# Kernel optimization log

Hardware: AMD Instinct MI355X
Metric: run time of the kernel (lower is better)

## Reference

```python
import jax, jax.numpy as jnp
import numpy as np

B, T, D = 4, 4096, 1024
H = 16
DK = D // H
EPS = 1e-6


def _phi(x):
    return jax.nn.elu(x) + 1.0


def setup_inputs() -> dict:
    key = jax.random.key(0)
    ks = jax.random.split(key, 9)
    s = 1.0 / np.sqrt(D)
    return {
        "x": jax.random.normal(ks[0], (B, T, D), dtype=jnp.float32),
        "Wq": jax.random.uniform(ks[1], (D, D), jnp.float32, -s, s),
        "bq": jax.random.uniform(ks[2], (D,), jnp.float32, -s, s),
        "Wk": jax.random.uniform(ks[3], (D, D), jnp.float32, -s, s),
        "bk": jax.random.uniform(ks[4], (D,), jnp.float32, -s, s),
        "Wv": jax.random.uniform(ks[5], (D, D), jnp.float32, -s, s),
        "bv": jax.random.uniform(ks[6], (D,), jnp.float32, -s, s),
        "Wo": jax.random.uniform(ks[7], (D, D), jnp.float32, -s, s),
        "bo": jax.random.uniform(ks[8], (D,), jnp.float32, -s, s),
    }


def reference(x, Wq, bq, Wk, bk, Wv, bv, Wo, bo):
    Bq, Tq, _ = x.shape

    def heads(y):  # [B,T,D] -> [B,H,T,DK]
        return y.reshape(Bq, Tq, H, DK).transpose(0, 2, 1, 3)

    q = _phi(heads(x @ Wq.T + bq))
    k = _phi(heads(x @ Wk.T + bk))
    v = heads(x @ Wv.T + bv)

    # associative KV summary: [B,H,DK,DK]
    kv = jnp.einsum("bhtd,bhtm->bhdm", k, v)
    # normalizer: q . (sum_t k + eps), then +eps, reciprocal
    z = 1.0 / (jnp.einsum("bhtd,bhd->bht", q, k.sum(axis=2) + EPS) + EPS)
    out = jnp.einsum("bhtd,bhdm,bht->bhtm", q, kv, z)

    out = out.transpose(0, 2, 1, 3).reshape(Bq, Tq, -1)  # [B,T,D]
    return out @ Wo.T + bo
```

## Files before the change

kernel.cpp:

```cpp
#include <hip/hip_runtime.h>
#include <cstdint>
#include <cstddef>

typedef unsigned short u16;
typedef __bf16 bf16x8 __attribute__((ext_vector_type(8)));
typedef float  f32x4  __attribute__((ext_vector_type(4)));
typedef u16    u16x8v __attribute__((ext_vector_type(8)));
typedef u16    u16x4  __attribute__((ext_vector_type(4)));

#define EPS 1e-6f

__device__ __forceinline__ u16 f2bf(float f) {
  union { float f; unsigned int u; } v; v.f = f;
  unsigned int u = v.u + 0x7FFFu + ((v.u >> 16) & 1u);
  return (u16)(u >> 16);
}
__device__ __forceinline__ float bf2f(u16 h) {
  union { unsigned int u; float f; } v; v.u = ((unsigned int)h) << 16;
  return v.f;
}
__device__ __forceinline__ void async16(const void* g, void* l) {
  __builtin_amdgcn_global_load_lds(
      (const __attribute__((address_space(1))) void*)g,
      (__attribute__((address_space(3))) void*)l, 16, 0, 0);
}

__global__ __launch_bounds__(256) void cvt_bf16_kernel(
    const float* __restrict__ in, u16* __restrict__ out, int n8) {
  int i = blockIdx.x * 256 + threadIdx.x;
  if (i >= n8) return;
  const float4* p = (const float4*)in;
  float4 a = p[2 * (size_t)i], b = p[2 * (size_t)i + 1];
  u16x8v o;
  o[0] = f2bf(a.x); o[1] = f2bf(a.y); o[2] = f2bf(a.z); o[3] = f2bf(a.w);
  o[4] = f2bf(b.x); o[5] = f2bf(b.y); o[6] = f2bf(b.z); o[7] = f2bf(b.w);
  *(u16x8v*)(out + 8 * (size_t)i) = o;
}

__global__ __launch_bounds__(256) void cvt_w_kernel(
    const float* __restrict__ w0, const float* __restrict__ w1,
    const float* __restrict__ w2, const float* __restrict__ w3,
    u16* __restrict__ o0, u16* __restrict__ o1,
    u16* __restrict__ o2, u16* __restrict__ o3) {
  const int gb = blockIdx.x;
  const float* in = (gb < 512) ? w0 : (gb < 1024) ? w1 : (gb < 1536) ? w2 : w3;
  u16* out = (gb < 512) ? o0 : (gb < 1024) ? o1 : (gb < 1536) ? o2 : o3;
  const int i = (gb & 511) * 256 + threadIdx.x;
  const float4* p = (const float4*)in;
  float4 a = p[2 * (size_t)i], b = p[2 * (size_t)i + 1];
  u16x8v o;
  o[0] = f2bf(a.x); o[1] = f2bf(a.y); o[2] = f2bf(a.z); o[3] = f2bf(a.w);
  o[4] = f2bf(b.x); o[5] = f2bf(b.y); o[6] = f2bf(b.z); o[7] = f2bf(b.w);
  *(u16x8v*)(out + 8 * (size_t)i) = o;
}

template <int MODE>
__global__ __launch_bounds__(512) void gemm2p(
    const u16* __restrict__ A, const u16* __restrict__ Bw,
    const float* __restrict__ bias0, const float* __restrict__ bias1,
    const float* __restrict__ bias2,
    u16* __restrict__ O0, u16* __restrict__ O1, u16* __restrict__ O2,
    float* __restrict__ Of, int K) {
  __shared__ u16 sA[2][256 * 64];
  __shared__ u16 sB[2][256 * 64];

  const int tid  = threadIdx.x;
  const int wave = tid >> 6;
  const int lane = tid & 63;
  const int bm = blockIdx.x * 256;
  const int bn = blockIdx.y * 256;
  const int wm = (wave >> 2) * 128;
  const int wn = (wave & 3) * 64;

  f32x4 acc[8][4] = {};

  const int srow = tid >> 3;
  const int sch8 = ((tid & 7) ^ ((tid >> 3) & 7)) * 8;
  const u16* gA0 = A  + (size_t)(bm + srow) * K + sch8;
  const u16* gB0 = Bw + (size_t)(bn + srow) * K + sch8;
  const int dwb = wave * 8 * 64;

#define STAGE2P(buf, k0)                                           \
  {                                                                \
    _Pragma("unroll")                                              \
    for (int s = 0; s < 4; s++) {                                  \
      async16(gA0 + (size_t)(k0) + (size_t)s * 64 * K,             \
              &sA[buf][s * 64 * 64 + dwb]);                        \
      async16(gB0 + (size_t)(k0) + (size_t)s * 64 * K,             \
              &sB[buf][s * 64 * 64 + dwb]);                        \
    }                                                              \
  }

  const int l15 = lane & 15, l4 = lane >> 4, l7 = lane & 7;

  STAGE2P(0, 0);
  __syncthreads();

  int cur = 0;
  const int NT = K >> 6;
  for (int t = 0; t < NT; ++t) {
    if (t + 1 < NT) STAGE2P(cur ^ 1, (t + 1) * 64);
#pragma unroll
    for (int kk = 0; kk < 2; kk++) {
      const int slot = ((kk * 4 + l4) ^ l7) * 8;
      bf16x8 af[8], bfv[4];
#pragma unroll
      for (int i = 0; i < 8; i++)
        af[i] = *(const bf16x8*)&sA[cur][(wm + i * 16 + l15) * 64 + slot];
#pragma unroll
      for (int n = 0; n < 4; n++)
        bfv[n] = *(const bf16x8*)&sB[cur][(wn + n * 16 + l15) * 64 + slot];
#pragma unroll
      for (int mi = 0; mi < 8; mi++)
#pragma unroll
        for (int ni = 0; ni < 4; ni++)
          acc[mi][ni] = __builtin_amdgcn_mfma_f32_16x16x32_bf16(
              af[mi], bfv[ni], acc[mi][ni], 0, 0, 0);
    }
    __syncthreads();
    cur ^= 1;
  }
#undef STAGE2P

  const int r0 = (lane >> 4) * 4, cc = lane & 15;
  if constexpr (MODE == 1) {
    const int mat = blockIdx.y >> 2;
    u16* outp = (mat == 0) ? O0 : (mat == 1) ? O1 : O2;
    const float* bias = (mat == 0) ? bias0 : (mat == 1) ? bias1 : bias2;
    const int act = (mat < 2);
    const int colb = (blockIdx.y & 3) * 256;
#pragma unroll
    for (int ni = 0; ni < 4; ni++) {
      const int col = colb + wn + ni * 16 + cc;
      const float bv = bias[col];
#pragma unroll
      for (int mi = 0; mi < 8; mi++) {
#pragma unroll
        for (int j = 0; j < 4; j++) {
          const int row = bm + wm + mi * 16 + r0 + j;
          float val = acc[mi][ni][j] + bv;
          if (act) val = (val > 0.f) ? (val + 1.f) : __expf(val);
          outp[(size_t)row * 1024 + col] = f2bf(val);
        }
      }
    }
  } else {
#pragma unroll
    for (int ni = 0; ni < 4; ni++) {
      const int col = bn + wn + ni * 16 + cc;
      const float bv = bias0[col];
#pragma unroll
      for (int mi = 0; mi < 8; mi++) {
#pragma unroll
        for (int j = 0; j < 4; j++) {
          const int row = bm + wm + mi * 16 + r0 + j;
          Of[(size_t)row * 1024 + col] = acc[mi][ni][j] + bv;
        }
      }
    }
  }
}

__global__ __launch_bounds__(256) void kv_mfma_kernel(
    const u16* __restrict__ Kb, const u16* __restrict__ Vb,
    float* __restrict__ kv, float* __restrict__ ksum) {
  const int bh = blockIdx.y;
  const int chunk = blockIdx.x;
  const int b = bh >> 4, h = bh & 15;
  const int tid = threadIdx.x, wave = tid >> 6, lane = tid & 63;

  __shared__ u16 sKT[64 * 64];
  __shared__ u16 sVT[64 * 64];

  f32x4 acc[4] = {};
  f32x4 accs[4] = {};

  union { u16x8v u; bf16x8 b; } uo;
#pragma unroll
  for (int e = 0; e < 8; e++) uo.u[e] = 0x3F80;
  const bf16x8 ones = uo.b;

  const int half = tid >> 7;
  const int j    = tid & 127;
  const int tg   = j >> 3;
  const int dg   = j & 7;
  const u16* src = half ? Vb : Kb;
  u16* dst = half ? sVT : sKT;
  const int colb = (4 * tg + 8 * dg) & 63;

  const size_t rowBase = (size_t)b * 4096 + (size_t)chunk * 512;
  const size_t gbase = (rowBase + 4 * tg) * 1024 + (size_t)h * 64 + dg * 8;

  u16x8v pre[2][4];
#pragma unroll
  for (int s = 0; s < 4; s++)
    pre[0][s] = *(const u16x8v*)(src + gbase + (size_t)s * 1024);

#pragma unroll
  for (int st = 0; st < 8; st++) {
    const int cb = st & 1;
    __syncthreads();
#pragma unroll
    for (int e = 0; e < 8; e++) {
      u16x4 w;
      w[0] = pre[cb][0][e]; w[1] = pre[cb][1][e];
      w[2] = pre[cb][2][e]; w[3] = pre[cb][3][e];
      *(u16x4*)&dst[(dg * 8 + e) * 64 + colb] = w;
    }
    if (st + 1 < 8) {
      const size_t nb = gbase + (size_t)(st + 1) * 64 * 1024;
#pragma unroll
      for (int s = 0; s < 4; s++)
        pre[cb ^ 1][s] = *(const u16x8v*)(src + nb + (size_t)s * 1024);
    }
    __syncthreads();

#pragma unroll
    for (int kst = 0; kst < 2; kst++) {
      const int q8 = kst * 32 + (lane >> 4) * 8;
      bf16x8 bfrag;
      {
        const int rr = wave * 16 + (lane & 15);
        const int c = (q8 + 8 * (rr >> 3)) & 63;
        bfrag = *(const bf16x8*)&sVT[rr * 64 + c];
      }
#pragma unroll
      for (int i = 0; i < 4; i++) {
        const int rr = i * 16 + (lane & 15);
        const int c = (q8 + 8 * (rr >> 3)) & 63;
        const bf16x8 afrag = *(const bf16x8*)&sKT[rr * 64 + c];
        acc[i] = __builtin_amdgcn_mfma_f32_16x16x32_bf16(afrag, bfrag, acc[i], 0, 0, 0);
        if (wave == 0)
          accs[i] = __builtin_amdgcn_mfma_f32_16x16x32_bf16(afrag, ones, accs[i], 0, 0, 0);
      }
    }
  }

  const int r0 = (lane >> 4) * 4, cc = lane & 15;
  float* kvp = kv + (size_t)bh * 4096;
#pragma unroll
  for (int i = 0; i < 4; i++)
#pragma unroll
    for (int jj = 0; jj < 4; jj++)
      atomicAdd(&kvp[(size_t)(i * 16 + r0 + jj) * 64 + wave * 16 + cc], acc[i][jj]);
  if (wave == 0 && cc == 0) {
#pragma unroll
    for (int i = 0; i < 4; i++)
#pragma unroll
      for (int jj = 0; jj < 4; jj++)
        atomicAdd(&ksum[(size_t)bh * 64 + i * 16 + r0 + jj], accs[i][jj]);
  }
}

#define QST 80
__global__ __launch_bounds__(256) void attn_apply_kernel(
    const u16* __restrict__ Qb, const float* __restrict__ kv,
    const float* __restrict__ ksum, u16* __restrict__ attn) {
  const int bh = blockIdx.y;
  const int tt = blockIdx.x;
  const int b = bh >> 4, h = bh & 15;
  const int tid = threadIdx.x, wave = tid >> 6, lane = tid & 63;

  __shared__ u16 skvT[64 * QST];
  __shared__ u16 sq[64 * QST];
  __shared__ float sz[64];
  __shared__ float sks[64];

  if (tid < 64) sks[tid] = ksum[(size_t)bh * 64 + tid] + EPS;

  const float* kvp = kv + (size_t)bh * 4096;
  for (int i = tid; i < 4096; i += 256) {
    const int dd = i >> 6, mm = i & 63;
    skvT[mm * QST + dd] = f2bf(kvp[i]);
  }
  const size_t qbase = ((size_t)b * 4096 + (size_t)tt * 64) * 1024 + h * 64;
  for (int i = tid; i < 4096; i += 256) {
    const int r = i >> 6, dd = i & 63;
    sq[r * QST + dd] = Qb[qbase + (size_t)r * 1024 + dd];
  }
  __syncthreads();

  if (tid < 64) {
    float za = 0.f;
#pragma unroll
    for (int j = 0; j < 64; j++) {
      const int dd = (j + tid) & 63;
      za += bf2f(sq[tid * QST + dd]) * sks[dd];
    }
    sz[tid] = 1.f / (za + EPS);
  }
  __syncthreads();

  f32x4 acc[4] = {};
#pragma unroll
  for (int ks2 = 0; ks2 < 2; ks2++) {
    const bf16x8 a = *(const bf16x8*)&sq[(wave * 16 + (lane & 15)) * QST + ks2 * 32 + (lane >> 4) * 8];
#pragma unroll
    for (int ni = 0; ni < 4; ni++) {
      const bf16x8 bv = *(const bf16x8*)&skvT[(ni * 16 + (lane & 15)) * QST + ks2 * 32 + (lane >> 4) * 8];
      acc[ni] = __builtin_amdgcn_mfma_f32_16x16x32_bf16(a, bv, acc[ni], 0, 0, 0);
    }
  }

  const int r0 = (lane >> 4) * 4, cc = lane & 15;
#pragma unroll
  for (int ni = 0; ni < 4; ni++) {
#pragma unroll
    for (int j = 0; j < 4; j++) {
      const int r = wave * 16 + r0 + j;
      const int c = ni * 16 + cc;
      const float val = acc[ni][j] * sz[r];
      attn[qbase + (size_t)r * 1024 + c] = f2bf(val);
    }
  }
}

extern "C" void kernel_launch(void* const* d_in, const int* in_sizes, int n_in,
                              void* d_out, int out_size, void* d_ws, size_t ws_size,
                              hipStream_t stream) {
  (void)in_sizes; (void)n_in; (void)out_size; (void)ws_size;
  const float* x  = (const float*)d_in[0];
  const float* Wq = (const float*)d_in[1];
  const float* bq = (const float*)d_in[2];
  const float* Wk = (const float*)d_in[3];
  const float* bk = (const float*)d_in[4];
  const float* Wv = (const float*)d_in[5];
  const float* bv = (const float*)d_in[6];
  const float* Wo = (const float*)d_in[7];
  const float* bo = (const float*)d_in[8];

  char* ws = (char*)d_ws;
  u16* xb    = (u16*)ws;  ws += 33554432;
  u16* wqkvb = (u16*)ws;  ws += 6291456;
  u16* wob   = (u16*)ws;  ws += 2097152;
  u16* Vb    = (u16*)ws;  ws += 33554432;
  u16* attn  = (u16*)ws;  ws += 33554432;
  float* kvb  = (float*)ws; ws += 1048576;
  float* ksum = (float*)ws; ws += 16384;

  u16* Qb = (u16*)d_out;
  u16* Kb = Qb + 16777216;

  hipMemsetAsync(kvb, 0, 1048576 + 16384, stream);

  cvt_bf16_kernel<<<8192, 256, 0, stream>>>(x, xb, 2097152);
  cvt_w_kernel<<<2048, 256, 0, stream>>>(Wq, Wk, Wv, Wo,
                                         wqkvb, wqkvb + 1048576, wqkvb + 2097152, wob);

  gemm2p<1><<<dim3(64, 12), 512, 0, stream>>>(
      xb, wqkvb, bq, bk, bv, Qb, Kb, Vb, nullptr, 1024);

  kv_mfma_kernel<<<dim3(8, 64), dim3(256), 0, stream>>>(Kb, Vb, kvb, ksum);
  attn_apply_kernel<<<dim3(64, 64), dim3(256), 0, stream>>>(Qb, kvb, ksum, attn);

  gemm2p<0><<<dim3(64, 4), 512, 0, stream>>>(
      attn, wob, bo, nullptr, nullptr, nullptr, nullptr, nullptr,
      (float*)d_out, 1024);
}
```

Baseline: 367.4 us.

## Rewrite GEMM main loop as 8-phase quadrant pipeline with interleaved async loads

Replaces the double-buffered GEMM loop with an 8-phase schedule. Each 256x256 tile is split into quadrant sub-tiles, and async global-to-LDS loads for the next k-steps are spread between the MFMA phases, with explicit vmcnt waits, barriers and setprio around MFMA bursts. The aim is to hide global load latency and reduce LDS read stalls by keeping fewer fragments live and overlapping loads with compute. It also changes the wave-to-tile mapping and reorders the epilogue stores. This adds complex hand-managed synchronization that could stall or be wrong if the wait counts are off, and it assumes K is a multiple of 128.

```diff
diff --git a/kernel.cpp b/kernel.cpp
--- a/kernel.cpp
+++ b/kernel.cpp
@@ -55,7 +55,7 @@
 }
 
 template <int MODE>
-__global__ __launch_bounds__(512) void gemm2p(
+__global__ __launch_bounds__(512) void gemm8p(
     const u16* __restrict__ A, const u16* __restrict__ Bw,
     const float* __restrict__ bias0, const float* __restrict__ bias1,
     const float* __restrict__ bias2,
@@ -64,97 +64,144 @@
   __shared__ u16 sA[2][256 * 64];
   __shared__ u16 sB[2][256 * 64];
 
-  const int tid  = threadIdx.x;
-  const int wave = tid >> 6;
-  const int lane = tid & 63;
-  const int bm = blockIdx.x * 256;
-  const int bn = blockIdx.y * 256;
-  const int wm = (wave >> 2) * 128;
+  const int tid = threadIdx.x, wave = tid >> 6, lane = tid & 63;
+  const int bm = blockIdx.x * 256, bn = blockIdx.y * 256;
+  const int wmh = (wave >> 2) * 64;
+  const int wq  = (wave & 3) * 32;
+  const int l15 = lane & 15, l4 = lane >> 4, l7 = lane & 7;
+
+  f32x4 acc[8][4] = {};
+
+  const int trow = tid >> 3;
+  const int sch8 = ((tid & 7) ^ (trow & 7)) * 8;
+
+#define STG_A(buf, qm, s, kt)                                                 \
+  async16(A + (size_t)(bm + (s)*128 + (qm)*64 + trow) * K + (kt) + sch8,      \
+          &sA[buf][(((qm)*128 + (s)*64) + wave * 8) * 64])
+#define STG_B(buf, qn, s, kt)                                                 \
+  async16(Bw + (size_t)(bn + ((s)*2 + (trow >> 5)) * 64 + (qn)*32 +           \
+                        (trow & 31)) * K + (kt) + sch8,                       \
+          &sB[buf][(((qn)*128 + (s)*64) + wave * 8) * 64])
+
+  bf16x8 af[4][2], bq[2][2];
+
+#define PH_READS(buf, qm, qn)                                                 \
+  _Pragma("unroll") for (int m = 0; m < 4; m++)                               \
+    _Pragma("unroll") for (int kk = 0; kk < 2; kk++)                          \
+      af[m][kk] = *(const bf16x8*)&sA[buf][((qm)*128 + wmh + m * 16 + l15) * 64 \
+                                           + ((kk * 4 + l4) ^ l7) * 8];       \
+  _Pragma("unroll") for (int n = 0; n < 2; n++)                               \
+    _Pragma("unroll") for (int kk = 0; kk < 2; kk++)                          \
+      bq[n][kk] = *(const bf16x8*)&sB[buf][((qn)*128 + wq + n * 16 + l15) * 64 \
+                                           + ((kk * 4 + l4) ^ l7) * 8];
+
+#define PH_MFMA(qm, qn)                                                       \
+  __builtin_amdgcn_s_barrier();                                               \
+  asm volatile("s_waitcnt lgkmcnt(0)" ::: "memory");                          \
+  __builtin_amdgcn_s_setprio(1);                                              \
+  _Pragma("unroll") for (int kk = 0; kk < 2; kk++)                            \
+    _Pragma("unroll") for (int m = 0; m < 4; m++)                             \
+      _Pragma("unroll") for (int n = 0; n < 2; n++)                           \
+        acc[(qm)*4 + m][(qn)*2 + n] = __builtin_amdgcn_mfma_f32_16x16x32_bf16(\
+            af[m][kk], bq[n][kk], acc[(qm)*4 + m][(qn)*2 + n], 0, 0, 0);      \
+  __builtin_amdgcn_s_setprio(0);                                              \
+  __builtin_amdgcn_s_barrier();                                               \
+  asm volatile("" ::: "memory");
+
+  STG_A(0, 0, 0, 0);  STG_A(0, 0, 1, 0);
+  STG_B(0, 0, 0, 0);  STG_B(0, 0, 1, 0);
+  STG_A(0, 1, 0, 0);  STG_A(0, 1, 1, 0);
+  STG_B(0, 1, 0, 0);  STG_B(0, 1, 1, 0);
+  STG_A(1, 0, 0, 64); STG_A(1, 0, 1, 64);
+  STG_B(1, 0, 0, 64); STG_B(1, 0, 1, 64);
+  asm volatile("s_waitcnt vmcnt(4)" ::: "memory");
+  __builtin_amdgcn_s_barrier();
+  asm volatile("" ::: "memory");
+
+  const int NT = K >> 6;
+  const int NI = NT >> 1;
+  for (int i = 0; i < NI; ++i) {
+    const int kO  = (2 * i + 1) * 64;
+    const int kE2 = (2 * i + 2) * 64;
+    const int kO2 = (2 * i + 3) * 64;
+    const bool gE2 = (2 * i + 2) < NT;
+    const bool gO2 = (2 * i + 3) < NT;
+
+    PH_READS(0, 0, 0);
+    STG_A(1, 1, 0, kO); STG_A(1, 1, 1, kO);
+    PH_MFMA(0, 0);
+    PH_READS(0, 0, 1);
+    STG_B(1, 1, 0, kO); STG_B(1, 1, 1, kO);
+    PH_MFMA(0, 1);
+    PH_READS(0, 1, 0);
+    if (gE2) { STG_A(0, 0, 0, kE2); STG_A(0, 0, 1, kE2); }
+    PH_MFMA(1, 0);
+    PH_READS(0, 1, 1);
+    if (gE2) {
+      STG_B(0, 0, 0, kE2); STG_B(0, 0, 1, kE2);
+      asm volatile("s_waitcnt vmcnt(4)" ::: "memory");
+    } else {
+      asm volatile("s_waitcnt vmcnt(0)" ::: "memory");
+    }
+    PH_MFMA(1, 1);
+    PH_READS(1, 0, 0);
+    if (gE2) { STG_A(0, 1, 0, kE2); STG_A(0, 1, 1, kE2); }
+    PH_MFMA(0, 0);
+    PH_READS(1, 0, 1);
+    if (gE2) { STG_B(0, 1, 0, kE2); STG_B(0, 1, 1, kE2); }
+    PH_MFMA(0, 1);
+    PH_READS(1, 1, 0);
+    if (gO2) { STG_A(1, 0, 0, kO2); STG_A(1, 0, 1, kO2); }
+    PH_MFMA(1, 0);
+    PH_READS(1, 1, 1);
+    if (gO2) { STG_B(1, 0, 0, kO2); STG_B(1, 0, 1, kO2); }
+    asm volatile("s_waitcnt vmcnt(4)" ::: "memory");
+    PH_MFMA(1, 1);
+  }
+#undef STG_A
+#undef STG_B
+#undef PH_READS
+#undef PH_MFMA
+
+  const int wm = wmh * 2;
   const int wn = (wave & 3) * 64;
-
-  f32x4 acc[8][4] = {};
-
-  const int srow = tid >> 3;
-  const int sch8 = ((tid & 7) ^ ((tid >> 3) & 7)) * 8;
-  const u16* gA0 = A  + (size_t)(bm + srow) * K + sch8;
-  const u16* gB0 = Bw + (size_t)(bn + srow) * K + sch8;
-  const int dwb = wave * 8 * 64;
-
-#define STAGE2P(buf, k0)                                           \
-  {                                                                \
-    _Pragma("unroll")                                              \
-    for (int s = 0; s < 4; s++) {                                  \
-      async16(gA0 + (size_t)(k0) + (size_t)s * 64 * K,             \
-              &sA[buf][s * 64 * 64 + dwb]);                        \
-      async16(gB0 + (size_t)(k0) + (size_t)s * 64 * K,             \
-              &sB[buf][s * 64 * 64 + dwb]);                        \
-    }                                                              \
-  }
-
-  const int l15 = lane & 15, l4 = lane >> 4, l7 = lane & 7;
-
-  STAGE2P(0, 0);
-  __syncthreads();
-
-  int cur = 0;
-  const int NT = K >> 6;
-  for (int t = 0; t < NT; ++t) {
-    if (t + 1 < NT) STAGE2P(cur ^ 1, (t + 1) * 64);
-#pragma unroll
-    for (int kk = 0; kk < 2; kk++) {
-      const int slot = ((kk * 4 + l4) ^ l7) * 8;
-      bf16x8 af[8], bfv[4];
-#pragma unroll
-      for (int i = 0; i < 8; i++)
-        af[i] = *(const bf16x8*)&sA[cur][(wm + i * 16 + l15) * 64 + slot];
-#pragma unroll
-      for (int n = 0; n < 4; n++)
-        bfv[n] = *(const bf16x8*)&sB[cur][(wn + n * 16 + l15) * 64 + slot];
-#pragma unroll
-      for (int mi = 0; mi < 8; mi++)
-#pragma unroll
-        for (int ni = 0; ni < 4; ni++)
-          acc[mi][ni] = __builtin_amdgcn_mfma_f32_16x16x32_bf16(
-              af[mi], bfv[ni], acc[mi][ni], 0, 0, 0);
-    }
-    __syncthreads();
-    cur ^= 1;
-  }
-#undef STAGE2P
-
-  const int r0 = (lane >> 4) * 4, cc = lane & 15;
+  const int r0 = l4 * 4, cc = l15;
   if constexpr (MODE == 1) {
     const int mat = blockIdx.y >> 2;
     u16* outp = (mat == 0) ? O0 : (mat == 1) ? O1 : O2;
     const float* bias = (mat == 0) ? bias0 : (mat == 1) ? bias1 : bias2;
     const int act = (mat < 2);
     const int colb = (blockIdx.y & 3) * 256;
-#pragma unroll
-    for (int ni = 0; ni < 4; ni++) {
-      const int col = colb + wn + ni * 16 + cc;
-      const float bv = bias[col];
-#pragma unroll
-      for (int mi = 0; mi < 8; mi++) {
-#pragma unroll
-        for (int j = 0; j < 4; j++) {
-          const int row = bm + wm + mi * 16 + r0 + j;
-          float val = acc[mi][ni][j] + bv;
+    float bvv[4];
+#pragma unroll
+    for (int ni = 0; ni < 4; ni++) bvv[ni] = bias[colb + wn + ni * 16 + cc];
+#pragma unroll
+    for (int mi = 0; mi < 8; mi++) {
+#pragma unroll
+      for (int j = 0; j < 4; j++) {
+        const int row = bm + wm + mi * 16 + r0 + j;
+#pragma unroll
+        for (int ni = 0; ni < 4; ni++) {
+          const int col = colb + wn + ni * 16 + cc;
+          float val = acc[mi][ni][j] + bvv[ni];
           if (act) val = (val > 0.f) ? (val + 1.f) : __expf(val);
           outp[(size_t)row * 1024 + col] = f2bf(val);
         }
       }
     }
   } else {
-#pragma unroll
-    for (int ni = 0; ni < 4; ni++) {
-      const int col = bn + wn + ni * 16 + cc;
-      const float bv = bias0[col];
-#pragma unroll
-      for (int mi = 0; mi < 8; mi++) {
-#pragma unroll
-        for (int j = 0; j < 4; j++) {
-          const int row = bm + wm + mi * 16 + r0 + j;
-          Of[(size_t)row * 1024 + col] = acc[mi][ni][j] + bv;
+    float bvv[4];
+#pragma unroll
+    for (int ni = 0; ni < 4; ni++) bvv[ni] = bias0[bn + wn + ni * 16 + cc];
+#pragma unroll
+    for (int mi = 0; mi < 8; mi++) {
+#pragma unroll
+      for (int j = 0; j < 4; j++) {
+        const int row = bm + wm + mi * 16 + r0 + j;
+#pragma unroll
+        for (int ni = 0; ni < 4; ni++) {
+          const int col = bn + wn + ni * 16 + cc;
+          Of[(size_t)row * 1024 + col] = acc[mi][ni][j] + bvv[ni];
         }
       }
     }
@@ -347,13 +394,13 @@
   cvt_w_kernel<<<2048, 256, 0, stream>>>(Wq, Wk, Wv, Wo,
                                          wqkvb, wqkvb + 1048576, wqkvb + 2097152, wob);
 
-  gemm2p<1><<<dim3(64, 12), 512, 0, stream>>>(
+  gemm8p<1><<<dim3(64, 12), 512, 0, stream>>>(
       xb, wqkvb, bq, bk, bv, Qb, Kb, Vb, nullptr, 1024);
 
   kv_mfma_kernel<<<dim3(8, 64), dim3(256), 0, stream>>>(Kb, Vb, kvb, ksum);
   attn_apply_kernel<<<dim3(64, 64), dim3(256), 0, stream>>>(Qb, kvb, ksum, attn);
 
-  gemm2p<0><<<dim3(64, 4), 512, 0, stream>>>(
+  gemm8p<0><<<dim3(64, 4), 512, 0, stream>>>(
       attn, wob, bo, nullptr, nullptr, nullptr, nullptr, nullptr,
       (float*)d_out, 1024);
 }
```

After: 338.0 us. -8.0%, faster.
